# Kernel optimization log

Measured on AMD Instinct MI355X. Metric: run time of the kernel, lower is better.

The kernel has to match this reference:

```python
import jax, jax.numpy as jnp
import numpy as np

N, B, E, H = 2048, 4, 256, 8
DH = E // H


def setup_inputs() -> dict:
    key = jax.random.key(0)
    ks = jax.random.split(key, 10)
    s = 1.0 / np.sqrt(E)
    f = lambda k, sh, sc=1.0: (jax.random.normal(k, sh, jnp.float32) * sc)
    return {
        "x": f(ks[0], (N, B, E)),
        "query_pos": f(ks[1], (N, B, E), 0.1),
        "receiver_val_res": f(ks[2], (N, B, E), 0.1),
        "sender_val_res": f(ks[3], (N, B, E), 0.1),
        "Wq": f(ks[4], (E, E), s), "bq": jnp.zeros((E,), jnp.float32),
        "Wk": f(ks[5], (E, E), s), "bk": jnp.zeros((E,), jnp.float32),
        "Wr": f(ks[6], (E, E), s), "br": jnp.zeros((E,), jnp.float32),
        "Ws": f(ks[7], (E, E), s), "bs_v": jnp.zeros((E,), jnp.float32),
        "Wo": f(ks[8], (E, E), s), "bo": jnp.zeros((E,), jnp.float32),
    }


def reference(x, query_pos, receiver_val_res, sender_val_res,
              Wq, bq, Wk, bk, Wr, br, Ws, bs_v, Wo, bo):
    # wrapper: key = query = x; key_pos = query_pos (same shape); residual = x
    q_in = x + query_pos  # [N,B,E]
    scale = 1.0 / np.sqrt(DH)
    q = (q_in @ Wq + bq).reshape(N, B, H, DH)
    k = (q_in @ Wk + bk).reshape(N, B, H, DH)
    # TIE edge-value decomposition: per-particle receiver/sender value tokens,
    # with accumulated cross-layer value residuals added.
    vr = q_in @ Wr + br + receiver_val_res  # [N,B,E]
    vs = q_in @ Ws + bs_v + sender_val_res  # [N,B,E]
    scores = jnp.einsum('nbhd,mbhd->bhnm', q, k) * scale  # [B,H,N,N]
    attn = jax.nn.softmax(scores, axis=-1)
    # out_i = sum_j a_ij (vr_i + vs_j) = vr_i + sum_j a_ij vs_j  (rows sum to 1)
    ctx = jnp.einsum('bhnm,mbhd->nbhd', attn, vs.reshape(N, B, H, DH))
    ctx = ctx + vr.reshape(N, B, H, DH)
    out = ctx.reshape(N, B, E) @ Wo + bo
    return (x + out, vr, vs)
```

## Files before the change

kernel.cpp:

```cpp
#include <hip/hip_runtime.h>
#include <hip/hip_bf16.h>

#define NTOK 2048
#define BATCH 4
#define EMB 256
#define NH 8
#define DHD 32
#define MROWS (NTOK*BATCH)
#define NBE (MROWS*EMB)

typedef __attribute__((ext_vector_type(8))) __bf16 bf16x8;
typedef __attribute__((ext_vector_type(4))) float f32x4;
typedef __attribute__((ext_vector_type(8))) unsigned short ushort8;
typedef __attribute__((ext_vector_type(4))) unsigned int uint4v;

__device__ __forceinline__ unsigned short f2bf(float f){
  unsigned int u = __builtin_bit_cast(unsigned int, f);
  u += 0x7fffu + ((u >> 16) & 1u);
  return (unsigned short)(u >> 16);
}
__device__ __forceinline__ float fexp2(float x){
#if __has_builtin(__builtin_amdgcn_exp2f)
  return __builtin_amdgcn_exp2f(x);
#else
  return exp2f(x);
#endif
}

#define QSC (0.17677669529663687f * 1.4426950408889634f)


__global__ __launch_bounds__(256) void k_add(const float* __restrict__ x,
                                             const float* __restrict__ qp,
                                             unsigned short* __restrict__ qpk){
  int t = blockIdx.x * 256 + threadIdx.x;
  int ppos = t * 8;
  int tile = ppos >> 12;
  int rem  = ppos & 4095;
  int kc   = rem >> 9;
  int row  = (rem >> 5) & 15;
  int kk   = rem & 31;
  int src  = (tile*16 + row)*256 + kc*32 + kk;
  f32x4 a0 = *(const f32x4*)(x + src);
  f32x4 a1 = *(const f32x4*)(x + src + 4);
  f32x4 b0 = *(const f32x4*)(qp + src);
  f32x4 b1 = *(const f32x4*)(qp + src + 4);
  ushort8 o;
#pragma unroll
  for (int j = 0; j < 4; ++j){
    o[j]   = f2bf(a0[j] + b0[j]);
    o[j+4] = f2bf(a1[j] + b1[j]);
  }
  *(ushort8*)(qpk + ppos) = o;
}

__global__ __launch_bounds__(256) void k_transW(const float* __restrict__ s0,
                                                const float* __restrict__ s1,
                                                const float* __restrict__ s2,
                                                const float* __restrict__ s3,
                                                const float* __restrict__ s4,
                                                unsigned short* __restrict__ wt){
  const float* srcs[5] = {s0, s1, s2, s3, s4};
  __shared__ float lds[64][65];
  int wi = blockIdx.z;
  int k0 = blockIdx.x * 64;
  int n0 = blockIdx.y * 64;
  int tid = threadIdx.x;
  const float* src = srcs[wi];
#pragma unroll
  for (int p = 0; p < 4; ++p){
    int r = p*16 + (tid>>4);
    int c = (tid&15)*4;
    f32x4 v = *(const f32x4*)(src + (k0+r)*256 + n0 + c);
#pragma unroll
    for (int j = 0; j < 4; ++j) lds[r][c+j] = v[j];
  }
  __syncthreads();
#pragma unroll
  for (int p = 0; p < 4; ++p){
    int nr = p*16 + (tid>>4);
    int kc = (tid&15)*4;
    unsigned long long pk = 0;
#pragma unroll
    for (int j = 0; j < 4; ++j)
      pk |= ((unsigned long long)f2bf(lds[kc+j][nr])) << (16*j);
    int n_g = n0 + nr, k_g = k0 + kc;
    int pos = (n_g>>4)*4096 + (k_g>>5)*512 + (n_g&15)*32 + (k_g&31);
    *(unsigned long long*)(wt + wi*65536 + pos) = pk;
  }
}

__global__ __launch_bounds__(256) void k_proj(const unsigned short* __restrict__ qpk,
                                              const unsigned short* __restrict__ wt,
                                              const float* __restrict__ bq,
                                              const float* __restrict__ bk,
                                              const float* __restrict__ br,
                                              const float* __restrict__ bs,
                                              const float* __restrict__ recv,
                                              const float* __restrict__ send,
                                              unsigned short* __restrict__ qbuf,
                                              unsigned short* __restrict__ kpk,
                                              float* __restrict__ vrout,
                                              float* __restrict__ vsout){
  int m0 = blockIdx.x * 64;
  int gc = blockIdx.y * 64;
  int widx = gc >> 8;
  int c0 = gc & 255;
  int tid = threadIdx.x;
  int w = tid >> 6, lane = tid & 63;
  int lr = lane & 15, lg = lane >> 4;

  __shared__ __align__(16) float shmemF[64*68];

  const unsigned short* apk = qpk + (m0/16 + w)*4096 + lr*32 + lg*8;
  const unsigned short* bpk = wt + widx*65536 + (c0/16)*4096 + lr*32 + lg*8;

  f32x4 acc[4];
#pragma unroll
  for (int f = 0; f < 4; ++f) acc[f] = (f32x4){0.f, 0.f, 0.f, 0.f};

#pragma unroll
  for (int k0 = 0; k0 < 256; k0 += 32){
    int kb = (k0 >> 5) * 512;
    bf16x8 af = *(const bf16x8*)(apk + kb);
#pragma unroll
    for (int f = 0; f < 4; ++f){
      bf16x8 bfrag = *(const bf16x8*)(bpk + f*4096 + kb);
      acc[f] = __builtin_amdgcn_mfma_f32_16x16x32_bf16(af, bfrag, acc[f], 0, 0, 0);
    }
  }

  const float* bias = (widx == 0) ? bq : (widx == 1) ? bk : (widx == 2) ? br : bs;

  if (widx <= 1){
    unsigned short (*st)[16][72] = (unsigned short(*)[16][72])shmemF;
#pragma unroll
    for (int f = 0; f < 4; ++f){
#pragma unroll
      for (int i = 0; i < 4; ++i){
        int c = c0 + f*16 + lr;
        float v = acc[f][i] + bias[c];
        st[w][lg*4+i][f*16+lr] = f2bf(widx == 0 ? v * QSC : v);
      }
    }
    if (widx == 0){
      int r = lane >> 2, co = (lane & 3) * 16;
      ushort8 a0 = *(ushort8*)&st[w][r][co];
      ushort8 a1 = *(ushort8*)&st[w][r][co + 8];
      unsigned short* dst = qbuf + (m0 + w*16 + r) * 256 + c0 + co;
      *(ushort8*)dst = a0;
      *(ushort8*)(dst + 8) = a1;
    } else {
      int cid = lane >> 3, s = lane & 7;
      int bb = cid >> 1, hr = cid & 1;
      int toko = s >> 1, dp = (s & 1) * 16;
      ushort8 a0 = *(ushort8*)&st[w][toko*4 + bb][hr*32 + dp];
      ushort8 a1 = *(ushort8*)&st[w][toko*4 + bb][hr*32 + dp + 8];
      int h  = (c0 >> 5) + hr;
      int n0 = (m0 + w*16) >> 2;
      int t0 = n0 & 63;
      int p0 = (((t0>>5)&1)<<4) + (((t0>>2)&1)<<5) + (((t0>>3)&3)<<2);
      unsigned short* dst = kpk + (bb*8 + h)*65536 + ((n0 & ~63) + p0 + toko)*32 + dp;
      *(ushort8*)dst = a0;
      *(ushort8*)(dst + 8) = a1;
    }
  } else {
    float (*ldsF)[68] = (float(*)[68])shmemF;
#pragma unroll
    for (int f = 0; f < 4; ++f){
#pragma unroll
      for (int i = 0; i < 4; ++i){
        ldsF[w*16 + lg*4 + i][f*16 + lr] = acc[f][i] + bias[c0 + f*16 + lr];
      }
    }
    __syncthreads();
    const float* gsrc = (widx == 2) ? recv : send;
    float* gdst = (widx == 2) ? vrout : vsout;
#pragma unroll
    for (int k = 0; k < 4; ++k){
      int chunk = k*256 + tid;
      int r = chunk >> 4;
      int cc = (chunk & 15) * 4;
      int idx = (m0 + r)*256 + c0 + cc;
      f32x4 v = *(const f32x4*)&ldsF[r][cc];
      f32x4 g = *(const f32x4*)(gsrc + idx);
#pragma unroll
      for (int j = 0; j < 4; ++j) v[j] += g[j];
      *(f32x4*)(gdst + idx) = v;
    }
  }
}

__global__ __launch_bounds__(256) void k_transV(const float* __restrict__ vsout,
                                                unsigned short* __restrict__ vpk){
  __shared__ float ldsT[32][129];
  int kv0 = blockIdx.x * 128;
  int bh = blockIdx.y;
  int b = bh >> 3, h = bh & 7;
  int tid = threadIdx.x;
#pragma unroll
  for (int p = 0; p < 4; ++p){
    int kvr = p*32 + (tid>>3);
    int dch = (tid&7)*4;
    f32x4 v = *(const f32x4*)(vsout + ((kv0 + kvr)*4 + b)*256 + h*32 + dch);
#pragma unroll
    for (int j = 0; j < 4; ++j) ldsT[dch+j][kvr] = v[j];
  }
  __syncthreads();
#pragma unroll
  for (int rep = 0; rep < 2; ++rep){
    int chunk = rep*256 + tid;
    int d   = chunk & 31;
    int sub = (chunk >> 5) & 3;
    int blk = chunk >> 7;
    int kvb = blk*32 + sub*8;
    ushort8 o;
#pragma unroll
    for (int j = 0; j < 8; ++j) o[j] = f2bf(ldsT[d][kvb + j]);
    *(ushort8*)(vpk + (bh*64 + (kv0>>5) + blk)*1024 + sub*256 + d*8) = o;
  }
}

__global__ __launch_bounds__(256) void k_attn(const unsigned short* __restrict__ qbuf,
                                              const unsigned short* __restrict__ kpk,
                                              const unsigned short* __restrict__ vpk,
                                              const float* __restrict__ vrbuf,
                                              unsigned short* __restrict__ ctx){
  int bid = blockIdx.x;
  int bh  = (bid & 7) + ((bid >> 8) << 3);
  int qt0 = ((bid >> 3) & 31) * 64;
  int b = bh >> 3, h = bh & 7;
  int tid = threadIdx.x;
  int w = tid >> 6, lane = tid & 63;
  int wq = w & 1;
  int wk = w >> 1;
  int lr = lane & 15, lg = lane >> 4;
  int lg4 = lg * 4;

  __shared__ float part[2][2][64][9];

  int qbase = qt0 + wq*32;
  bf16x8 qfA = *(const bf16x8*)(qbuf + ((qbase + lr)*BATCH + b)*EMB + h*DHD + lg*8);
  bf16x8 qfB = *(const bf16x8*)(qbuf + ((qbase + 16 + lr)*BATCH + b)*EMB + h*DHD + lg*8);

  const unsigned short* kbase = kpk + bh*65536 + wk*(1024*32) + lr*32 + lg*8;
  const unsigned short* vbase = vpk + bh*65536 + wk*(32*1024) + lg*256 + lr*8;

  f32x4 accA0 = (f32x4){0.f,0.f,0.f,0.f};
  f32x4 accA1 = (f32x4){0.f,0.f,0.f,0.f};
  f32x4 accB0 = (f32x4){0.f,0.f,0.f,0.f};
  f32x4 accB1 = (f32x4){0.f,0.f,0.f,0.f};
  float lsumA = 0.f, lsumB = 0.f;

  bf16x8 kA[4], vA[4], kB[4], vB[4];

  auto loadfr = [&](int kv0, bf16x8* kf, bf16x8* vf){
#pragma unroll
    for (int j = 0; j < 4; ++j)
      kf[j] = *(const bf16x8*)(kbase + (kv0 + j*16)*32);
#pragma unroll
    for (int c = 0; c < 2; ++c)
#pragma unroll
      for (int dh = 0; dh < 2; ++dh)
        vf[c*2+dh] = *(const bf16x8*)(vbase + ((kv0>>5) + c)*1024 + dh*128);
  };

  auto tile_compute = [&](const bf16x8* kf, const bf16x8* vf){
    f32x4 z = (f32x4){0.f,0.f,0.f,0.f};
    f32x4 sA[4], sB[4];
#pragma unroll
    for (int j = 0; j < 4; ++j){
      sA[j] = __builtin_amdgcn_mfma_f32_16x16x32_bf16(kf[j], qfA, z, 0, 0, 0);
      sB[j] = __builtin_amdgcn_mfma_f32_16x16x32_bf16(kf[j], qfB, z, 0, 0, 0);
    }

    float pA[4][4], pB[4][4];
    float psA = 0.f, psB = 0.f;
#pragma unroll
    for (int j = 0; j < 4; ++j){
#pragma unroll
      for (int i = 0; i < 4; ++i){
        pA[j][i] = fexp2(sA[j][i]);
        pB[j][i] = fexp2(sB[j][i]);
      }
      psA += (pA[j][0] + pA[j][1]) + (pA[j][2] + pA[j][3]);
      psB += (pB[j][0] + pB[j][1]) + (pB[j][2] + pB[j][3]);
    }
    lsumA += psA;
    lsumB += psB;

#pragma unroll
    for (int c = 0; c < 2; ++c){
      uint4v dA, dB;
      dA[0] = __builtin_amdgcn_perm(__builtin_bit_cast(unsigned int, pA[c][1]),
                                    __builtin_bit_cast(unsigned int, pA[c][0]), 0x07060302u);
      dA[1] = __builtin_amdgcn_perm(__builtin_bit_cast(unsigned int, pA[c][3]),
                                    __builtin_bit_cast(unsigned int, pA[c][2]), 0x07060302u);
      dA[2] = __builtin_amdgcn_perm(__builtin_bit_cast(unsigned int, pA[c+2][1]),
                                    __builtin_bit_cast(unsigned int, pA[c+2][0]), 0x07060302u);
      dA[3] = __builtin_amdgcn_perm(__builtin_bit_cast(unsigned int, pA[c+2][3]),
                                    __builtin_bit_cast(unsigned int, pA[c+2][2]), 0x07060302u);
      bf16x8 pfA = __builtin_bit_cast(bf16x8, dA);
      accA0 = __builtin_amdgcn_mfma_f32_16x16x32_bf16(pfA, vf[c*2+0], accA0, 0, 0, 0);
      accA1 = __builtin_amdgcn_mfma_f32_16x16x32_bf16(pfA, vf[c*2+1], accA1, 0, 0, 0);
      dB[0] = __builtin_amdgcn_perm(__builtin_bit_cast(unsigned int, pB[c][1]),
                                    __builtin_bit_cast(unsigned int, pB[c][0]), 0x07060302u);
      dB[1] = __builtin_amdgcn_perm(__builtin_bit_cast(unsigned int, pB[c][3]),
                                    __builtin_bit_cast(unsigned int, pB[c][2]), 0x07060302u);
      dB[2] = __builtin_amdgcn_perm(__builtin_bit_cast(unsigned int, pB[c+2][1]),
                                    __builtin_bit_cast(unsigned int, pB[c+2][0]), 0x07060302u);
      dB[3] = __builtin_amdgcn_perm(__builtin_bit_cast(unsigned int, pB[c+2][3]),
                                    __builtin_bit_cast(unsigned int, pB[c+2][2]), 0x07060302u);
      bf16x8 pfB = __builtin_bit_cast(bf16x8, dB);
      accB0 = __builtin_amdgcn_mfma_f32_16x16x32_bf16(pfB, vf[c*2+0], accB0, 0, 0, 0);
      accB1 = __builtin_amdgcn_mfma_f32_16x16x32_bf16(pfB, vf[c*2+1], accB1, 0, 0, 0);
    }
  };

  loadfr(0, kA, vA);
  for (int t = 0; t < 16; t += 2){
    loadfr((t+1)*64, kB, vB);
    tile_compute(kA, vA);
    if (t + 2 < 16) loadfr((t+2)*64, kA, vA);
    tile_compute(kB, vB);
  }

  lsumA += __shfl_xor(lsumA, 16);
  lsumA += __shfl_xor(lsumA, 32);
  lsumB += __shfl_xor(lsumB, 16);
  lsumB += __shfl_xor(lsumB, 32);

  if (wk == 1){
#pragma unroll
    for (int i = 0; i < 4; ++i){
      part[wq][0][lane][i]   = accA0[i];
      part[wq][0][lane][4+i] = accA1[i];
      part[wq][1][lane][i]   = accB0[i];
      part[wq][1][lane][4+i] = accB1[i];
    }
    part[wq][0][lane][8] = lsumA;
    part[wq][1][lane][8] = lsumB;
  }
  __syncthreads();
  if (wk == 0){
#pragma unroll
    for (int i = 0; i < 4; ++i){
      accA0[i] += part[wq][0][lane][i];
      accA1[i] += part[wq][0][lane][4+i];
      accB0[i] += part[wq][1][lane][i];
      accB1[i] += part[wq][1][lane][4+i];
    }
    lsumA += part[wq][0][lane][8];
    lsumB += part[wq][1][lane][8];
    float invA = 1.0f / lsumA;
    float invB = 1.0f / lsumB;
#pragma unroll
    for (int i = 0; i < 4; ++i){
      float vinvA = __shfl(invA, lg4 + i);
      float vinvB = __shfl(invB, lg4 + i);
      int qA = qbase + lg4 + i;
      int mA = qA*4 + b;
      int idxA = mA*256 + h*DHD + lr;
      int posA = (qA>>2)*4096 + h*512 + (4*(qA&3)+b)*32 + lr;
      ctx[posA]      = f2bf(accA0[i] * vinvA + vrbuf[idxA]);
      ctx[posA + 16] = f2bf(accA1[i] * vinvA + vrbuf[idxA + 16]);
      int qB = qbase + 16 + lg4 + i;
      int mB = qB*4 + b;
      int idxB = mB*256 + h*DHD + lr;
      int posB = (qB>>2)*4096 + h*512 + (4*(qB&3)+b)*32 + lr;
      ctx[posB]      = f2bf(accB0[i] * vinvB + vrbuf[idxB]);
      ctx[posB + 16] = f2bf(accB1[i] * vinvB + vrbuf[idxB + 16]);
    }
  }
}

__global__ __launch_bounds__(256) void k_out(const unsigned short* __restrict__ ctx,
                                             const unsigned short* __restrict__ wt,
                                             const float* __restrict__ bo,
                                             const float* __restrict__ x,
                                             float* __restrict__ out0){
  int m0 = blockIdx.x * 64;
  int c0 = blockIdx.y * 64;
  int tid = threadIdx.x;
  int w = tid >> 6, lane = tid & 63;
  int lr = lane & 15, lg = lane >> 4;

  __shared__ __align__(16) float ldsF[64][68];

  const unsigned short* apk = ctx + (m0/16 + w)*4096 + lr*32 + lg*8;
  const unsigned short* bpk = wt + 4*65536 + (c0/16)*4096 + lr*32 + lg*8;

  f32x4 acc[4];
#pragma unroll
  for (int f = 0; f < 4; ++f) acc[f] = (f32x4){0.f, 0.f, 0.f, 0.f};

#pragma unroll
  for (int k0 = 0; k0 < 256; k0 += 32){
    int kb = (k0 >> 5) * 512;
    bf16x8 af = *(const bf16x8*)(apk + kb);
#pragma unroll
    for (int f = 0; f < 4; ++f){
      bf16x8 bfrag = *(const bf16x8*)(bpk + f*4096 + kb);
      acc[f] = __builtin_amdgcn_mfma_f32_16x16x32_bf16(af, bfrag, acc[f], 0, 0, 0);
    }
  }

#pragma unroll
  for (int f = 0; f < 4; ++f){
#pragma unroll
    for (int i = 0; i < 4; ++i){
      ldsF[w*16 + lg*4 + i][f*16 + lr] = acc[f][i] + bo[c0 + f*16 + lr];
    }
  }
  __syncthreads();
#pragma unroll
  for (int k = 0; k < 4; ++k){
    int chunk = k*256 + tid;
    int r = chunk >> 4;
    int cc = (chunk & 15) * 4;
    int idx = (m0 + r)*256 + c0 + cc;
    f32x4 v = *(const f32x4*)&ldsF[r][cc];
    f32x4 g = *(const f32x4*)(x + idx);
#pragma unroll
    for (int j = 0; j < 4; ++j) v[j] += g[j];
    *(f32x4*)(out0 + idx) = v;
  }
}

extern "C" void kernel_launch(void* const* d_in, const int* in_sizes, int n_in,
                              void* d_out, int out_size, void* d_ws, size_t ws_size,
                              hipStream_t stream){
  const float* x    = (const float*)d_in[0];
  const float* qp   = (const float*)d_in[1];
  const float* recv = (const float*)d_in[2];
  const float* send = (const float*)d_in[3];
  const float* Wq   = (const float*)d_in[4];
  const float* bq   = (const float*)d_in[5];
  const float* Wk   = (const float*)d_in[6];
  const float* bk   = (const float*)d_in[7];
  const float* Wr   = (const float*)d_in[8];
  const float* br   = (const float*)d_in[9];
  const float* Wsv  = (const float*)d_in[10];
  const float* bsv  = (const float*)d_in[11];
  const float* Wo   = (const float*)d_in[12];
  const float* bo   = (const float*)d_in[13];

  float* out0  = (float*)d_out;
  float* vrout = out0 + NBE;
  float* vsout = out0 + 2*NBE;

  unsigned short* ws   = (unsigned short*)d_ws;
  unsigned short* qin  = ws;
  unsigned short* qbuf = ws + NBE;
  unsigned short* kpk  = ws + 2*NBE;
  unsigned short* vpk  = ws + 3*NBE;
  unsigned short* wt   = ws + 4*NBE;

  hipLaunchKernelGGL(k_add, dim3(NBE/8/256), dim3(256), 0, stream, x, qp, qin);
  hipLaunchKernelGGL(k_transW, dim3(4, 4, 5), dim3(256), 0, stream, Wq, Wk, Wr, Wsv, Wo, wt);
  hipLaunchKernelGGL(k_proj, dim3(128, 16), dim3(256), 0, stream,
                     qin, wt, bq, bk, br, bsv, recv, send, qbuf, kpk, vrout, vsout);
  hipLaunchKernelGGL(k_transV, dim3(16, 32), dim3(256), 0, stream, vsout, vpk);
  hipLaunchKernelGGL(k_attn, dim3(1024), dim3(256), 0, stream,
                     qbuf, kpk, vpk, vrout, qin );
  hipLaunchKernelGGL(k_out, dim3(128, 4), dim3(256), 0, stream,
                     qin , wt, bo, x, out0);
}
```

Baseline: 81.25 us.

## Split attention KV range across four waves, each covering all 64 queries

Each wave now processes all four 16-query fragments of the 64-query tile over one quarter of the KV sequence, instead of a 2x2 split of queries by KV halves. Every loaded K/V fragment is reused across four query fragments instead of two, which halves per-wave K/V global loads and the KV loop length. The cost is more accumulator registers per wave and a larger three-way partial reduction through shared memory, done serially by wave 0.

```diff
diff --git a/kernel.cpp b/kernel.cpp
--- a/kernel.cpp
+++ b/kernel.cpp
@@ -232,25 +232,26 @@
   int b = bh >> 3, h = bh & 7;
   int tid = threadIdx.x;
   int w = tid >> 6, lane = tid & 63;
-  int wq = w & 1;
-  int wk = w >> 1;
   int lr = lane & 15, lg = lane >> 4;
   int lg4 = lg * 4;
 
-  __shared__ float part[2][2][64][9];
-
-  int qbase = qt0 + wq*32;
-  bf16x8 qfA = *(const bf16x8*)(qbuf + ((qbase + lr)*BATCH + b)*EMB + h*DHD + lg*8);
-  bf16x8 qfB = *(const bf16x8*)(qbuf + ((qbase + 16 + lr)*BATCH + b)*EMB + h*DHD + lg*8);
-
-  const unsigned short* kbase = kpk + bh*65536 + wk*(1024*32) + lr*32 + lg*8;
-  const unsigned short* vbase = vpk + bh*65536 + wk*(32*1024) + lg*256 + lr*8;
-
-  f32x4 accA0 = (f32x4){0.f,0.f,0.f,0.f};
-  f32x4 accA1 = (f32x4){0.f,0.f,0.f,0.f};
-  f32x4 accB0 = (f32x4){0.f,0.f,0.f,0.f};
-  f32x4 accB1 = (f32x4){0.f,0.f,0.f,0.f};
-  float lsumA = 0.f, lsumB = 0.f;
+  __shared__ float part[3][4][64][9];
+
+  bf16x8 qf[4];
+#pragma unroll
+  for (int f = 0; f < 4; ++f)
+    qf[f] = *(const bf16x8*)(qbuf + ((qt0 + f*16 + lr)*BATCH + b)*EMB + h*DHD + lg*8);
+
+  const unsigned short* kbase = kpk + bh*65536 + w*16384 + lr*32 + lg*8;
+  const unsigned short* vbase = vpk + bh*65536 + w*16384 + lg*256 + lr*8;
+
+  f32x4 acc[4][2];
+#pragma unroll
+  for (int f = 0; f < 4; ++f){
+    acc[f][0] = (f32x4){0.f,0.f,0.f,0.f};
+    acc[f][1] = (f32x4){0.f,0.f,0.f,0.f};
+  }
+  float lsum[4] = {0.f, 0.f, 0.f, 0.f};
 
   bf16x8 kA[4], vA[4], kB[4], vB[4];
 
@@ -267,109 +268,91 @@
 
   auto tile_compute = [&](const bf16x8* kf, const bf16x8* vf){
     f32x4 z = (f32x4){0.f,0.f,0.f,0.f};
-    f32x4 sA[4], sB[4];
-#pragma unroll
-    for (int j = 0; j < 4; ++j){
-      sA[j] = __builtin_amdgcn_mfma_f32_16x16x32_bf16(kf[j], qfA, z, 0, 0, 0);
-      sB[j] = __builtin_amdgcn_mfma_f32_16x16x32_bf16(kf[j], qfB, z, 0, 0, 0);
-    }
-
-    float pA[4][4], pB[4][4];
-    float psA = 0.f, psB = 0.f;
-#pragma unroll
-    for (int j = 0; j < 4; ++j){
-#pragma unroll
-      for (int i = 0; i < 4; ++i){
-        pA[j][i] = fexp2(sA[j][i]);
-        pB[j][i] = fexp2(sB[j][i]);
-      }
-      psA += (pA[j][0] + pA[j][1]) + (pA[j][2] + pA[j][3]);
-      psB += (pB[j][0] + pB[j][1]) + (pB[j][2] + pB[j][3]);
-    }
-    lsumA += psA;
-    lsumB += psB;
-
-#pragma unroll
-    for (int c = 0; c < 2; ++c){
-      uint4v dA, dB;
-      dA[0] = __builtin_amdgcn_perm(__builtin_bit_cast(unsigned int, pA[c][1]),
-                                    __builtin_bit_cast(unsigned int, pA[c][0]), 0x07060302u);
-      dA[1] = __builtin_amdgcn_perm(__builtin_bit_cast(unsigned int, pA[c][3]),
-                                    __builtin_bit_cast(unsigned int, pA[c][2]), 0x07060302u);
-      dA[2] = __builtin_amdgcn_perm(__builtin_bit_cast(unsigned int, pA[c+2][1]),
-                                    __builtin_bit_cast(unsigned int, pA[c+2][0]), 0x07060302u);
-      dA[3] = __builtin_amdgcn_perm(__builtin_bit_cast(unsigned int, pA[c+2][3]),
-                                    __builtin_bit_cast(unsigned int, pA[c+2][2]), 0x07060302u);
-      bf16x8 pfA = __builtin_bit_cast(bf16x8, dA);
-      accA0 = __builtin_amdgcn_mfma_f32_16x16x32_bf16(pfA, vf[c*2+0], accA0, 0, 0, 0);
-      accA1 = __builtin_amdgcn_mfma_f32_16x16x32_bf16(pfA, vf[c*2+1], accA1, 0, 0, 0);
-      dB[0] = __builtin_amdgcn_perm(__builtin_bit_cast(unsigned int, pB[c][1]),
-                                    __builtin_bit_cast(unsigned int, pB[c][0]), 0x07060302u);
-      dB[1] = __builtin_amdgcn_perm(__builtin_bit_cast(unsigned int, pB[c][3]),
-                                    __builtin_bit_cast(unsigned int, pB[c][2]), 0x07060302u);
-      dB[2] = __builtin_amdgcn_perm(__builtin_bit_cast(unsigned int, pB[c+2][1]),
-                                    __builtin_bit_cast(unsigned int, pB[c+2][0]), 0x07060302u);
-      dB[3] = __builtin_amdgcn_perm(__builtin_bit_cast(unsigned int, pB[c+2][3]),
-                                    __builtin_bit_cast(unsigned int, pB[c+2][2]), 0x07060302u);
-      bf16x8 pfB = __builtin_bit_cast(bf16x8, dB);
-      accB0 = __builtin_amdgcn_mfma_f32_16x16x32_bf16(pfB, vf[c*2+0], accB0, 0, 0, 0);
-      accB1 = __builtin_amdgcn_mfma_f32_16x16x32_bf16(pfB, vf[c*2+1], accB1, 0, 0, 0);
+#pragma unroll
+    for (int f = 0; f < 4; ++f){
+      f32x4 s[4];
+#pragma unroll
+      for (int j = 0; j < 4; ++j)
+        s[j] = __builtin_amdgcn_mfma_f32_16x16x32_bf16(kf[j], qf[f], z, 0, 0, 0);
+
+      float p[4][4];
+      float ps = 0.f;
+#pragma unroll
+      for (int j = 0; j < 4; ++j){
+#pragma unroll
+        for (int i = 0; i < 4; ++i){
+          p[j][i] = fexp2(s[j][i]);
+        }
+        ps += (p[j][0] + p[j][1]) + (p[j][2] + p[j][3]);
+      }
+      lsum[f] += ps;
+
+#pragma unroll
+      for (int c = 0; c < 2; ++c){
+        uint4v d;
+        d[0] = __builtin_amdgcn_perm(__builtin_bit_cast(unsigned int, p[c][1]),
+                                     __builtin_bit_cast(unsigned int, p[c][0]), 0x07060302u);
+        d[1] = __builtin_amdgcn_perm(__builtin_bit_cast(unsigned int, p[c][3]),
+                                     __builtin_bit_cast(unsigned int, p[c][2]), 0x07060302u);
+        d[2] = __builtin_amdgcn_perm(__builtin_bit_cast(unsigned int, p[c+2][1]),
+                                     __builtin_bit_cast(unsigned int, p[c+2][0]), 0x07060302u);
+        d[3] = __builtin_amdgcn_perm(__builtin_bit_cast(unsigned int, p[c+2][3]),
+                                     __builtin_bit_cast(unsigned int, p[c+2][2]), 0x07060302u);
+        bf16x8 pf = __builtin_bit_cast(bf16x8, d);
+        acc[f][0] = __builtin_amdgcn_mfma_f32_16x16x32_bf16(pf, vf[c*2+0], acc[f][0], 0, 0, 0);
+        acc[f][1] = __builtin_amdgcn_mfma_f32_16x16x32_bf16(pf, vf[c*2+1], acc[f][1], 0, 0, 0);
+      }
     }
   };
 
   loadfr(0, kA, vA);
-  for (int t = 0; t < 16; t += 2){
+  for (int t = 0; t < 8; t += 2){
     loadfr((t+1)*64, kB, vB);
     tile_compute(kA, vA);
-    if (t + 2 < 16) loadfr((t+2)*64, kA, vA);
+    if (t + 2 < 8) loadfr((t+2)*64, kA, vA);
     tile_compute(kB, vB);
   }
 
-  lsumA += __shfl_xor(lsumA, 16);
-  lsumA += __shfl_xor(lsumA, 32);
-  lsumB += __shfl_xor(lsumB, 16);
-  lsumB += __shfl_xor(lsumB, 32);
-
-  if (wk == 1){
-#pragma unroll
-    for (int i = 0; i < 4; ++i){
-      part[wq][0][lane][i]   = accA0[i];
-      part[wq][0][lane][4+i] = accA1[i];
-      part[wq][1][lane][i]   = accB0[i];
-      part[wq][1][lane][4+i] = accB1[i];
-    }
-    part[wq][0][lane][8] = lsumA;
-    part[wq][1][lane][8] = lsumB;
+#pragma unroll
+  for (int f = 0; f < 4; ++f){
+    lsum[f] += __shfl_xor(lsum[f], 16);
+    lsum[f] += __shfl_xor(lsum[f], 32);
+  }
+
+  if (w > 0){
+#pragma unroll
+    for (int f = 0; f < 4; ++f){
+#pragma unroll
+      for (int i = 0; i < 4; ++i){
+        part[w-1][f][lane][i]   = acc[f][0][i];
+        part[w-1][f][lane][4+i] = acc[f][1][i];
+      }
+      part[w-1][f][lane][8] = lsum[f];
+    }
   }
   __syncthreads();
-  if (wk == 0){
-#pragma unroll
-    for (int i = 0; i < 4; ++i){
-      accA0[i] += part[wq][0][lane][i];
-      accA1[i] += part[wq][0][lane][4+i];
-      accB0[i] += part[wq][1][lane][i];
-      accB1[i] += part[wq][1][lane][4+i];
-    }
-    lsumA += part[wq][0][lane][8];
-    lsumB += part[wq][1][lane][8];
-    float invA = 1.0f / lsumA;
-    float invB = 1.0f / lsumB;
-#pragma unroll
-    for (int i = 0; i < 4; ++i){
-      float vinvA = __shfl(invA, lg4 + i);
-      float vinvB = __shfl(invB, lg4 + i);
-      int qA = qbase + lg4 + i;
-      int mA = qA*4 + b;
-      int idxA = mA*256 + h*DHD + lr;
-      int posA = (qA>>2)*4096 + h*512 + (4*(qA&3)+b)*32 + lr;
-      ctx[posA]      = f2bf(accA0[i] * vinvA + vrbuf[idxA]);
-      ctx[posA + 16] = f2bf(accA1[i] * vinvA + vrbuf[idxA + 16]);
-      int qB = qbase + 16 + lg4 + i;
-      int mB = qB*4 + b;
-      int idxB = mB*256 + h*DHD + lr;
-      int posB = (qB>>2)*4096 + h*512 + (4*(qB&3)+b)*32 + lr;
-      ctx[posB]      = f2bf(accB0[i] * vinvB + vrbuf[idxB]);
-      ctx[posB + 16] = f2bf(accB1[i] * vinvB + vrbuf[idxB + 16]);
+  if (w == 0){
+#pragma unroll
+    for (int f = 0; f < 4; ++f){
+#pragma unroll
+      for (int ww = 0; ww < 3; ++ww){
+#pragma unroll
+        for (int i = 0; i < 4; ++i){
+          acc[f][0][i] += part[ww][f][lane][i];
+          acc[f][1][i] += part[ww][f][lane][4+i];
+        }
+        lsum[f] += part[ww][f][lane][8];
+      }
+      float inv = 1.0f / lsum[f];
+#pragma unroll
+      for (int i = 0; i < 4; ++i){
+        float vinv = __shfl(inv, lg4 + i);
+        int q = qt0 + f*16 + lg4 + i;
+        int idx = (q*4 + b)*256 + h*DHD + lr;
+        int pos = (q>>2)*4096 + h*512 + (4*(q&3)+b)*32 + lr;
+        ctx[pos]      = f2bf(acc[f][0][i] * vinv + vrbuf[idx]);
+        ctx[pos + 16] = f2bf(acc[f][1][i] * vinv + vrbuf[idx + 16]);
+      }
     }
   }
 }
```

New measurement: 80.35 us. About the same (-1.1%).
